# Optimization experiments

Measured on AMD Instinct MI355X. Metric: run time of the kernel, lower is better.

The kernel has to match this reference:

```python
import jax, jax.numpy as jnp
import numpy as np

N_NODES = 100000

def setup_inputs() -> dict:
    key = jax.random.key(0)
    k1, k2, k3, k4 = jax.random.split(key, 4)
    B, S, D, H = 50000, 10, 128, 128
    nodes = jax.random.randint(k1, (B,), 0, N_NODES, dtype=jnp.int64 if jax.config.jax_enable_x64 else jnp.int32)
    neigh_idx = jax.random.randint(k2, (B, S), 0, N_NODES, dtype=nodes.dtype)
    feature = jax.random.normal(k3, (N_NODES, D), dtype=jnp.float32)
    weight = jax.random.normal(k4, (2 * D, H), dtype=jnp.float32) * (1.0 / np.sqrt(2 * D))
    return {"nodes": nodes, "neigh_idx": neigh_idx, "feature": feature, "weight": weight}

def reference(nodes, neigh_idx, feature, weight):
    # Mean aggregation over sampled neighbors: [B, S, D] -> [B, D]
    neigh_feats = jnp.mean(feature[neigh_idx], axis=1)
    # Self features: [B, D]
    self_feats = feature[nodes]
    # Concat + linear + ReLU (gcn=False branch)
    combined = jnp.concatenate([self_feats, neigh_feats], axis=1)  # [B, 2D]
    return jax.nn.relu(combined @ weight)  # [B, H]
```

## Files before the change

kernel.cpp:

```cpp
#include <hip/hip_runtime.h>


typedef __attribute__((ext_vector_type(8))) short bf16x8;
typedef __attribute__((ext_vector_type(4))) float f32x4;

__device__ __forceinline__ unsigned short f2bf(float x) {
  unsigned int u = __float_as_uint(x);
  u += 0x7fffu + ((u >> 16) & 1u);
  return (unsigned short)(u >> 16);
}

__global__ void sage_prep_wt(const float* __restrict__ W,
                             unsigned short* __restrict__ Wt) {
  int tid = blockIdx.x * blockDim.x + threadIdx.x;
  float4 v = ((const float4*)W)[tid];
  int flat = tid << 2;
  int k = flat >> 7;
  int h = flat & 127;
  Wt[(h + 0) * 256 + k] = f2bf(v.x);
  Wt[(h + 1) * 256 + k] = f2bf(v.y);
  Wt[(h + 2) * 256 + k] = f2bf(v.z);
  Wt[(h + 3) * 256 + k] = f2bf(v.w);
}

__global__ __launch_bounds__(512, 6)
void sage_fused3(const int* __restrict__ nodes,
                 const int* __restrict__ neigh,
                 const float* __restrict__ feat,
                 const unsigned short* __restrict__ Wt,
                 float* __restrict__ out, int B)
{
  constexpr int K = 256, H = 128, S = 10;
  constexpr int TILE = 32;
  constexpr int STR = K + 8;
  __shared__ unsigned short Clds[TILE * STR];

  const int t = threadIdx.x;
  const int block0 = blockIdx.x * TILE;

  {
    const int r   = t >> 4;
    const int sub = t & 15;
    const int b   = block0 + r;
    unsigned short* crow = &Clds[r * STR];
    if (b < B) {
      const float4* f4 = (const float4*)feat;
      const long srow = (long)nodes[b] * 32;
      float4 s0 = f4[srow + sub];
      float4 s1 = f4[srow + 16 + sub];

      float ax0=0.f, ay0=0.f, az0=0.f, aw0=0.f;
      float ax1=0.f, ay1=0.f, az1=0.f, aw1=0.f;
#pragma unroll
      for (int s = 0; s < S; ++s) {
        const long nrow = (long)neigh[b * S + s] * 32;
        float4 v0 = f4[nrow + sub];
        float4 v1 = f4[nrow + 16 + sub];
        ax0 += v0.x; ay0 += v0.y; az0 += v0.z; aw0 += v0.w;
        ax1 += v1.x; ay1 += v1.y; az1 += v1.z; aw1 += v1.w;
      }
      ushort4 o;
      o.x = f2bf(s0.x); o.y = f2bf(s0.y); o.z = f2bf(s0.z); o.w = f2bf(s0.w);
      *(ushort4*)&crow[4 * sub] = o;
      o.x = f2bf(s1.x); o.y = f2bf(s1.y); o.z = f2bf(s1.z); o.w = f2bf(s1.w);
      *(ushort4*)&crow[64 + 4 * sub] = o;
      o.x = f2bf(ax0 * 0.1f); o.y = f2bf(ay0 * 0.1f);
      o.z = f2bf(az0 * 0.1f); o.w = f2bf(aw0 * 0.1f);
      *(ushort4*)&crow[128 + 4 * sub] = o;
      o.x = f2bf(ax1 * 0.1f); o.y = f2bf(ay1 * 0.1f);
      o.z = f2bf(az1 * 0.1f); o.w = f2bf(aw1 * 0.1f);
      *(ushort4*)&crow[192 + 4 * sub] = o;
    } else {
      ushort4 z; z.x = z.y = z.z = z.w = 0;
      *(ushort4*)&crow[4 * sub] = z;
      *(ushort4*)&crow[64 + 4 * sub] = z;
      *(ushort4*)&crow[128 + 4 * sub] = z;
      *(ushort4*)&crow[192 + 4 * sub] = z;
    }
  }
  __syncthreads();
  __builtin_amdgcn_sched_barrier(0);

  const int lane = t & 63;
  const int wave = t >> 6;
  const int m    = lane & 15;
  const int quad = lane >> 4;
  const int cbase = wave * 16;

  bf16x8 bfrag[8];
#pragma unroll
  for (int ks = 0; ks < 8; ++ks)
    bfrag[ks] = *(const bf16x8*)&Wt[(cbase + m) * K + ks * 32 + quad * 8];

  f32x4 acc0 = {0.f, 0.f, 0.f, 0.f};
  f32x4 acc1 = {0.f, 0.f, 0.f, 0.f};
#pragma unroll
  for (int ks = 0; ks < 8; ++ks) {
    const int koff = ks * 32 + quad * 8;
    bf16x8 a0 = *(const bf16x8*)&Clds[(m     ) * STR + koff];
    bf16x8 a1 = *(const bf16x8*)&Clds[(16 + m) * STR + koff];
    acc0 = __builtin_amdgcn_mfma_f32_16x16x32_bf16(a0, bfrag[ks], acc0, 0, 0, 0);
    acc1 = __builtin_amdgcn_mfma_f32_16x16x32_bf16(a1, bfrag[ks], acc1, 0, 0, 0);
  }

#pragma unroll
  for (int reg = 0; reg < 4; ++reg) {
    const int row0 = quad * 4 + reg;
    const int gb0 = block0 + row0;
    const int gb1 = gb0 + 16;
    if (gb0 < B) out[(size_t)gb0 * H + cbase + m] = fmaxf(acc0[reg], 0.0f);
    if (gb1 < B) out[(size_t)gb1 * H + cbase + m] = fmaxf(acc1[reg], 0.0f);
  }
}

extern "C" void kernel_launch(void* const* d_in, const int* in_sizes, int n_in,
                              void* d_out, int out_size, void* d_ws, size_t ws_size,
                              hipStream_t stream) {
  const int*   nodes = (const int*)d_in[0];
  const int*   neigh = (const int*)d_in[1];
  const float* feat  = (const float*)d_in[2];
  const float* W     = (const float*)d_in[3];
  float*       out   = (float*)d_out;
  const int B = in_sizes[0];

  unsigned short* Wt = (unsigned short*)d_ws;
  sage_prep_wt<<<32, 256, 0, stream>>>(W, Wt);
  const int grid = (B + 31) / 32;
  sage_fused3<<<grid, 512, 0, stream>>>(nodes, neigh, feat, Wt, out, B);
}
```

Measured before the change: 130.1 us.

## Pre-convert feature table to bf16 and gather bf16 rows in fused kernel

Adds a pre-pass that converts the whole fp32 feature table to bf16 in workspace, and the fused kernel then gathers 256-byte bf16 rows instead of 512-byte fp32 rows. This halves gather traffic in the main kernel, which is meant to cut its memory-bound cost. In exchange every call pays a full read and write of the 51 MB table, even though only about 550k rows are gathered, and the neighbor mean is accumulated from bf16-rounded inputs. The weight transpose prep is also rewritten to go through an LDS tile so its global writes are coalesced, and an fp32 fallback is kept for small workspaces.

Result: slower. 136.4 us (+4.8%).

```diff
diff --git a/kernel.cpp b/kernel.cpp
--- a/kernel.cpp
+++ b/kernel.cpp
@@ -2,6 +2,7 @@
 
 
 typedef __attribute__((ext_vector_type(8))) short bf16x8;
+typedef __attribute__((ext_vector_type(8))) unsigned short u16x8;
 typedef __attribute__((ext_vector_type(4))) float f32x4;
 
 __device__ __forceinline__ unsigned short f2bf(float x) {
@@ -9,24 +10,57 @@
   u += 0x7fffu + ((u >> 16) & 1u);
   return (unsigned short)(u >> 16);
 }
-
-__global__ void sage_prep_wt(const float* __restrict__ W,
-                             unsigned short* __restrict__ Wt) {
-  int tid = blockIdx.x * blockDim.x + threadIdx.x;
-  float4 v = ((const float4*)W)[tid];
-  int flat = tid << 2;
-  int k = flat >> 7;
-  int h = flat & 127;
-  Wt[(h + 0) * 256 + k] = f2bf(v.x);
-  Wt[(h + 1) * 256 + k] = f2bf(v.y);
-  Wt[(h + 2) * 256 + k] = f2bf(v.z);
-  Wt[(h + 3) * 256 + k] = f2bf(v.w);
+__device__ __forceinline__ float b2f(unsigned short u) {
+  return __uint_as_float(((unsigned int)u) << 16);
+}
+
+__global__ void sage_prep_wt2(const float* __restrict__ W,
+                              unsigned short* __restrict__ Wt) {
+  __shared__ float tile[32][132];
+  const int t = threadIdx.x;
+  const int kbase = blockIdx.x * 32;
+  const float4* w4 = (const float4*)(W + (size_t)kbase * 128);
+#pragma unroll
+  for (int j = 0; j < 4; ++j) {
+    int f4i = t + j * 256;
+    float4 v = w4[f4i];
+    int flat = f4i << 2;
+    int kk = flat >> 7;
+    int h  = flat & 127;
+    tile[kk][h] = v.x; tile[kk][h + 1] = v.y;
+    tile[kk][h + 2] = v.z; tile[kk][h + 3] = v.w;
+  }
+  __syncthreads();
+  const int h  = t >> 1;
+  const int kc = (t & 1) * 16;
+  unsigned short* dst = &Wt[(size_t)h * 256 + kbase + kc];
+#pragma unroll
+  for (int j = 0; j < 4; ++j) {
+    ushort4 o;
+    o.x = f2bf(tile[kc + 4 * j + 0][h]);
+    o.y = f2bf(tile[kc + 4 * j + 1][h]);
+    o.z = f2bf(tile[kc + 4 * j + 2][h]);
+    o.w = f2bf(tile[kc + 4 * j + 3][h]);
+    *(ushort4*)&dst[4 * j] = o;
+  }
+}
+
+__global__ void sage_prep_feat(const float* __restrict__ feat,
+                               unsigned short* __restrict__ fb, int n8) {
+  int i = blockIdx.x * blockDim.x + threadIdx.x;
+  if (i >= n8) return;
+  const float4* f4 = (const float4*)feat;
+  float4 a = f4[2 * i], b = f4[2 * i + 1];
+  u16x8 o;
+  o[0] = f2bf(a.x); o[1] = f2bf(a.y); o[2] = f2bf(a.z); o[3] = f2bf(a.w);
+  o[4] = f2bf(b.x); o[5] = f2bf(b.y); o[6] = f2bf(b.z); o[7] = f2bf(b.w);
+  *(u16x8*)&fb[(size_t)i * 8] = o;
 }
 
 __global__ __launch_bounds__(512, 6)
-void sage_fused3(const int* __restrict__ nodes,
+void sage_fused7(const int* __restrict__ nodes,
                  const int* __restrict__ neigh,
-                 const float* __restrict__ feat,
+                 const unsigned short* __restrict__ fb,
                  const unsigned short* __restrict__ Wt,
                  float* __restrict__ out, int B)
 {
@@ -38,6 +72,86 @@
   const int t = threadIdx.x;
   const int block0 = blockIdx.x * TILE;
 
+  {
+    const int r   = t >> 4;
+    const int sub = t & 15;
+    const int b   = block0 + r;
+    unsigned short* crow = &Clds[r * STR];
+    if (b < B) {
+      const long soff = (long)nodes[b] * 128 + sub * 8;
+      u16x8 sv = *(const u16x8*)&fb[soff];
+
+      float a0 = 0.f, a1 = 0.f, a2 = 0.f, a3 = 0.f;
+      float a4 = 0.f, a5 = 0.f, a6 = 0.f, a7 = 0.f;
+#pragma unroll
+      for (int s = 0; s < S; ++s) {
+        const long noff = (long)neigh[b * S + s] * 128 + sub * 8;
+        u16x8 v = *(const u16x8*)&fb[noff];
+        a0 += b2f(v[0]); a1 += b2f(v[1]); a2 += b2f(v[2]); a3 += b2f(v[3]);
+        a4 += b2f(v[4]); a5 += b2f(v[5]); a6 += b2f(v[6]); a7 += b2f(v[7]);
+      }
+      *(u16x8*)&crow[8 * sub] = sv;
+      u16x8 o;
+      o[0] = f2bf(a0 * 0.1f); o[1] = f2bf(a1 * 0.1f);
+      o[2] = f2bf(a2 * 0.1f); o[3] = f2bf(a3 * 0.1f);
+      o[4] = f2bf(a4 * 0.1f); o[5] = f2bf(a5 * 0.1f);
+      o[6] = f2bf(a6 * 0.1f); o[7] = f2bf(a7 * 0.1f);
+      *(u16x8*)&crow[128 + 8 * sub] = o;
+    } else {
+      u16x8 z = {0, 0, 0, 0, 0, 0, 0, 0};
+      *(u16x8*)&crow[8 * sub] = z;
+      *(u16x8*)&crow[128 + 8 * sub] = z;
+    }
+  }
+  __syncthreads();
+  __builtin_amdgcn_sched_barrier(0);
+
+  const int lane = t & 63;
+  const int wave = t >> 6;
+  const int m    = lane & 15;
+  const int quad = lane >> 4;
+  const int cbase = wave * 16;
+
+  bf16x8 bfrag[8];
+#pragma unroll
+  for (int ks = 0; ks < 8; ++ks)
+    bfrag[ks] = *(const bf16x8*)&Wt[(cbase + m) * K + ks * 32 + quad * 8];
+
+  f32x4 acc0 = {0.f, 0.f, 0.f, 0.f};
+  f32x4 acc1 = {0.f, 0.f, 0.f, 0.f};
+#pragma unroll
+  for (int ks = 0; ks < 8; ++ks) {
+    const int koff = ks * 32 + quad * 8;
+    bf16x8 a0 = *(const bf16x8*)&Clds[(m     ) * STR + koff];
+    bf16x8 a1 = *(const bf16x8*)&Clds[(16 + m) * STR + koff];
+    acc0 = __builtin_amdgcn_mfma_f32_16x16x32_bf16(a0, bfrag[ks], acc0, 0, 0, 0);
+    acc1 = __builtin_amdgcn_mfma_f32_16x16x32_bf16(a1, bfrag[ks], acc1, 0, 0, 0);
+  }
+
+#pragma unroll
+  for (int reg = 0; reg < 4; ++reg) {
+    const int row0 = quad * 4 + reg;
+    const int gb0 = block0 + row0;
+    const int gb1 = gb0 + 16;
+    if (gb0 < B) out[(size_t)gb0 * H + cbase + m] = fmaxf(acc0[reg], 0.0f);
+    if (gb1 < B) out[(size_t)gb1 * H + cbase + m] = fmaxf(acc1[reg], 0.0f);
+  }
+}
+
+__global__ __launch_bounds__(512, 6)
+void sage_fused_fp32(const int* __restrict__ nodes,
+                     const int* __restrict__ neigh,
+                     const float* __restrict__ feat,
+                     const unsigned short* __restrict__ Wt,
+                     float* __restrict__ out, int B)
+{
+  constexpr int K = 256, H = 128, S = 10;
+  constexpr int TILE = 32;
+  constexpr int STR = K + 8;
+  __shared__ unsigned short Clds[TILE * STR];
+
+  const int t = threadIdx.x;
+  const int block0 = blockIdx.x * TILE;
   {
     const int r   = t >> 4;
     const int sub = t & 15;
@@ -48,7 +162,6 @@
       const long srow = (long)nodes[b] * 32;
       float4 s0 = f4[srow + sub];
       float4 s1 = f4[srow + 16 + sub];
-
       float ax0=0.f, ay0=0.f, az0=0.f, aw0=0.f;
       float ax1=0.f, ay1=0.f, az1=0.f, aw1=0.f;
 #pragma unroll
@@ -102,7 +215,6 @@
     acc0 = __builtin_amdgcn_mfma_f32_16x16x32_bf16(a0, bfrag[ks], acc0, 0, 0, 0);
     acc1 = __builtin_amdgcn_mfma_f32_16x16x32_bf16(a1, bfrag[ks], acc1, 0, 0, 0);
   }
-
 #pragma unroll
   for (int reg = 0; reg < 4; ++reg) {
     const int row0 = quad * 4 + reg;
@@ -121,10 +233,20 @@
   const float* feat  = (const float*)d_in[2];
   const float* W     = (const float*)d_in[3];
   float*       out   = (float*)d_out;
-  const int B = in_sizes[0];
+  const int B      = in_sizes[0];
+  const int nfeat  = in_sizes[2];
 
   unsigned short* Wt = (unsigned short*)d_ws;
-  sage_prep_wt<<<32, 256, 0, stream>>>(W, Wt);
+  sage_prep_wt2<<<8, 256, 0, stream>>>(W, Wt);
+
+  const size_t need = 65536 + (size_t)nfeat * 2;
   const int grid = (B + 31) / 32;
-  sage_fused3<<<grid, 512, 0, stream>>>(nodes, neigh, feat, Wt, out, B);
-}
+  if (ws_size >= need) {
+    unsigned short* fb = (unsigned short*)((char*)d_ws + 65536);
+    const int n8 = nfeat / 8;
+    sage_prep_feat<<<(n8 + 511) / 512, 512, 0, stream>>>(feat, fb, n8);
+    sage_fused7<<<grid, 512, 0, stream>>>(nodes, neigh, fb, Wt, out, B);
+  } else {
+    sage_fused_fp32<<<grid, 512, 0, stream>>>(nodes, neigh, feat, Wt, out, B);
+  }
+}
```
